# Optimization experiments

Measured on AMD Instinct MI355X. Metric: run time of the kernel, lower is better.

Reference implementation:

```python
import jax, jax.numpy as jnp
import numpy as np

B, T, P, H = 64, 64, 32, 256  # batch, seq_len, num_series, hidden


def setup_inputs() -> dict:
    key = jax.random.key(0)
    ks = jax.random.split(key, 16)
    s = 0.05  # weight init scale (keeps gates unsaturated, like PyTorch's 1/sqrt(H) init)
    return {
        'X': jax.random.normal(ks[0], (B, T, P), dtype=jnp.float32),
        'eps': jax.random.normal(ks[1], (1, B, H), dtype=jnp.float32),
        'W_ih_enc': jax.random.normal(ks[2], (3 * H, P), dtype=jnp.float32) * s,
        'W_hh_enc': jax.random.normal(ks[3], (3 * H, H), dtype=jnp.float32) * s,
        'b_ih_enc': jax.random.normal(ks[4], (3 * H,), dtype=jnp.float32) * s,
        'b_hh_enc': jax.random.normal(ks[5], (3 * H,), dtype=jnp.float32) * s,
        'fc_mu_w': jax.random.normal(ks[6], (H, H), dtype=jnp.float32) * s,
        'fc_mu_b': jax.random.normal(ks[7], (H,), dtype=jnp.float32) * s,
        'fc_std_w': jax.random.normal(ks[8], (H, H), dtype=jnp.float32) * s,
        'fc_std_b': jax.random.normal(ks[9], (H,), dtype=jnp.float32) * s,
        'W_ih_dec': jax.random.normal(ks[10], (P, 3 * H, P), dtype=jnp.float32) * s,
        'W_hh_dec': jax.random.normal(ks[11], (P, 3 * H, H), dtype=jnp.float32) * s,
        'b_ih_dec': jax.random.normal(ks[12], (P, 3 * H), dtype=jnp.float32) * s,
        'b_hh_dec': jax.random.normal(ks[13], (P, 3 * H), dtype=jnp.float32) * s,
        'lin_w': jax.random.normal(ks[14], (P, 1, H), dtype=jnp.float32) * s,
        'lin_b': jax.random.normal(ks[15], (P, 1), dtype=jnp.float32) * s,
    }


def _gru_scan(x_seq, h0, Wih, Whh, bih, bhh):
    """PyTorch-convention GRU over x_seq [B,T,in] with h0 [B,H]. Returns (h_last, hs [B,T,H])."""
    Hh = Whh.shape[1]
    # batch the input projection for all timesteps at once
    gi = jnp.einsum('bti,gi->btg', x_seq, Wih) + bih  # [B,T,3H]

    def step(h, gi_t):
        gh = h @ Whh.T + bhh
        r = jax.nn.sigmoid(gi_t[:, :Hh] + gh[:, :Hh])
        zg = jax.nn.sigmoid(gi_t[:, Hh:2 * Hh] + gh[:, Hh:2 * Hh])
        n = jnp.tanh(gi_t[:, 2 * Hh:] + r * gh[:, 2 * Hh:])
        h_new = (1.0 - zg) * n + zg * h
        return h_new, h_new

    h_last, hs = jax.lax.scan(step, h0, jnp.swapaxes(gi, 0, 1))
    return h_last, jnp.swapaxes(hs, 0, 1)


def reference(X, eps, W_ih_enc, W_hh_enc, b_ih_enc, b_hh_enc,
              fc_mu_w, fc_mu_b, fc_std_w, fc_std_b,
              W_ih_dec, W_hh_dec, b_ih_dec, b_hh_dec, lin_w, lin_b):
    # phase=0, mode='train'. Padded Xp = cat(zeros[:, :1], X); Xp[:,1:11] == X[:,0:10].
    Bb = X.shape[0]
    h0 = jnp.zeros((Bb, H), X.dtype)
    h_t, _ = _gru_scan(X[:, 0:10, :], h0, W_ih_enc, W_hh_enc, b_ih_enc, b_hh_enc)  # [B,H]
    mu = h_t @ fc_mu_w.T + fc_mu_b
    log_var = h_t @ fc_std_w.T + fc_std_b
    sigma = jnp.exp(0.5 * log_var)
    z = mu + sigma * eps[0]  # reparameterization; eps plays the role of torch.randn

    # decoder input: cat(Xp[:,0:1], Xp[:,11:-1]) == cat(zeros step, X[:,10:T-1])  -> [B, T-10, P]
    dec_in = jnp.concatenate([jnp.zeros_like(X[:, :1, :]), X[:, 10:-1, :]], axis=1)

    def one_series(Wih, Whh, bih, bhh, lw, lb):
        _, hs = _gru_scan(dec_in, z, Wih, Whh, bih, bhh)  # [B, T-10, H]
        return jnp.einsum('bth,oh->bto', hs, lw) + lb     # [B, T-10, 1]

    # connection is all-ones -> every decoder sees the full dec_in; vmap over stacked params
    pred = jax.vmap(one_series)(W_ih_dec, W_hh_dec, b_ih_dec, b_hh_dec, lin_w, lin_b)  # [P,B,T-10,1]
    return pred, log_var[None], mu[None]
```

## Files before the change

kernel.cpp:

```cpp
#include <hip/hip_runtime.h>

typedef unsigned int u32;
typedef unsigned short u16;
typedef __attribute__((ext_vector_type(8))) short short8;
typedef __attribute__((ext_vector_type(4))) float f32x4;

#define DEV static __device__ __forceinline__

DEV float b2f(u16 v){ union{u32 u; float f;} c; c.u = ((u32)v) << 16; return c.f; }
DEV u16 f2b(float f){ union{float ff; u32 u;} c; c.ff = f; return (u16)((c.u + 0x7fffu + ((c.u >> 16) & 1u)) >> 16); }
DEV float sigm(float x){ return 1.f/(1.f + __expf(-x)); }
DEV float tanh_(float x){ float e = __expf(-2.f*x); return (1.f-e)/(1.f+e); }

#define SER_STRIDE 221184

#define BLDS_U16 (48*3*64*8)
#define HA_U16   (2*2048)
#define XAB_U16  (2*256)
#define LWF_U16  256
#define SMEM_BYTES ((BLDS_U16 + HA_U16 + XAB_U16 + LWF_U16)*2)

DEV int hxi(int m, int c){ return (((c>>5)*32) + (((c>>3)&3)*8) + m)*8 + (c&7); }

__global__ __launch_bounds__(256) void pack_kernel(
    const float* __restrict__ WihD, const float* __restrict__ WhhD,
    const float* __restrict__ WihE, const float* __restrict__ WhhE,
    u16* __restrict__ wsB)
{
  const int ps = blockIdx.y;
  const int f  = blockIdx.x*4 + (threadIdx.x >> 6);
  const int n0 = f / 9, k = f - n0*9;
  const int lane = threadIdx.x & 63;
  const int n = lane & 15, q = lane >> 4;
  const int row = n0*16 + n;
  const float* Whh = (ps < 32) ? WhhD + ps*196608 : WhhE;
  const float* Wih = (ps < 32) ? WihD + ps*24576  : WihE;
  const float* src = (k < 8) ? (Whh + row*256 + k*32 + q*8) : (Wih + row*32 + q*8);
  u32 wd[4];
  #pragma unroll
  for (int j = 0; j < 4; ++j) {
    u16 lo = f2b(src[2*j]);
    u16 hi = f2b(src[2*j+1]);
    wd[j] = (u32)lo | ((u32)hi << 16);
  }
  *(uint4*)(wsB + (((size_t)ps*432 + f)*64 + lane)*8) = make_uint4(wd[0], wd[1], wd[2], wd[3]);
}

template<int NSTEPS, bool IS_DEC>
DEV void gru_body(u16* hA, u16* xA, u16* Blds, u16* lwfc,
                  const u16* __restrict__ Bp,
                  const float* __restrict__ bihP, const float* __restrict__ bhhP,
                  const float* __restrict__ X, const float* __restrict__ z0,
                  const float* __restrict__ lwp, const float* __restrict__ lbp,
                  float* __restrict__ predp, int b0)
{
  const int tid = threadIdx.x;
  const int w = tid >> 6, lane = tid & 63;
  const int n = lane & 15, q = lane >> 4;
  const int isel  = q >> 1;
  const int mbase = (q & 1) * 4;
  const int colS  = (2*w + isel)*16 + n;

  for (int idx = tid; idx < (HA_U16 + XAB_U16)/2; idx += 512)
    ((u32*)hA)[idx] = 0;
  __syncthreads();

  if (IS_DEC) {
    const int m = tid >> 6, c0 = (tid*4) & 255;
    float4 v = *(const float4*)&z0[(b0+m)*256 + c0];
    const int base = hxi(m, c0);
    hA[base]   = f2b(v.x); hA[base+1] = f2b(v.y);
    hA[base+2] = f2b(v.z); hA[base+3] = f2b(v.w);
  } else if (tid < 256) {
    const int m = tid >> 5, c = tid & 31;
    xA[((c>>3)*8 + m)*8 + (c&7)] = f2b(X[(b0+m)*2048 + c]);
  }
  if (IS_DEC && tid < 256)
    lwfc[tid] = f2b(lwp[tid]);

  #pragma unroll
  for (int r = 0; r < 18; ++r) {
    const int g = r*512 + tid;
    const int frag = g >> 6, e = g & 63;
    const int nt = frag / 3, kk = frag - nt*3;
    ((uint4*)Blds)[g] = ((const uint4*)Bp)[((size_t)nt*9 + 6 + kk)*64 + e];
  }

  short8 Bres[36];
  #pragma unroll
  for (int i = 0; i < 2; ++i)
    #pragma unroll
    for (int g = 0; g < 3; ++g)
      #pragma unroll
      for (int k = 0; k < 6; ++k)
        Bres[(i*3+g)*6 + k] =
          *(const short8*)(Bp + (((size_t)(g*16 + 2*w + i)*9 + k)*64 + lane)*8);
  #pragma unroll
  for (int r = 0; r < 36; ++r)
    asm volatile("" : "+v"(Bres[r]));

  const float brS  = bihP[colS]     + bhhP[colS];
  const float bzS  = bihP[256+colS] + bhhP[256+colS];
  const float bnxS = bihP[512+colS];
  const float bnhS = bhhP[512+colS];
  const float lb = IS_DEC ? lbp[0] : 0.f;

  float hold[4];
  #pragma unroll
  for (int rr = 0; rr < 4; ++rr)
    hold[rr] = IS_DEC ? b2f(f2b(z0[(b0 + mbase + rr)*256 + colS])) : 0.f;

  const int wbase = hxi(mbase, colS);
  __syncthreads();

  #pragma unroll 1
  for (int t = 0; t < NSTEPS; ++t) {
    const int par = t & 1;
    u16* hP = hA + par*2048;

    float xv = 0.f;
    const bool doX = (t+1 < NSTEPS) && (tid < 256);
    const int xm = tid >> 5, xc = tid & 31;
    if (doX) xv = X[(b0+xm)*2048 + (IS_DEC ? (t+10) : (t+1))*32 + xc];

    short8 af[9];
    #pragma unroll
    for (int k0 = 0; k0 < 8; ++k0)
      af[k0] = *(const short8*)&hP[(k0*32 + q*8 + (n&7))*8];
    af[8] = *(const short8*)&xA[par*256 + (q*8 + (n&7))*8];

    if (IS_DEC && w == 0 && t > 0) {
      f32x4 lp = {0,0,0,0};
      #pragma unroll
      for (int k0 = 0; k0 < 8; ++k0) {
        const short8 lf = *(const short8*)&lwfc[(k0*4 + q)*8];
        lp = __builtin_amdgcn_mfma_f32_16x16x32_bf16(af[k0], lf, lp, 0,0,0);
      }
      if (n == 0 && q < 2) {
        #pragma unroll
        for (int rr = 0; rr < 4; ++rr)
          predp[(b0 + q*4 + rr)*54 + (t-1)] = lp[rr] + lb;
      }
    }

    if (doX) xA[(par^1)*256 + ((xc>>3)*8 + xm)*8 + (xc&7)] = f2b(xv);

    f32x4 accr[2], accz[2], accnh[2], accnx[2];
    #pragma unroll
    for (int i = 0; i < 2; ++i) {
      const int ntr = 2*w + i, ntz = 16 + 2*w + i, ntn = 32 + 2*w + i;
      f32x4 ar={0,0,0,0}, az={0,0,0,0}, anh={0,0,0,0}, anx={0,0,0,0};
      const short8 b6r = *(const short8*)&Blds[((ntr*3+0)*64+lane)*8];
      const short8 b7r = *(const short8*)&Blds[((ntr*3+1)*64+lane)*8];
      const short8 b8r = *(const short8*)&Blds[((ntr*3+2)*64+lane)*8];
      const short8 b6z = *(const short8*)&Blds[((ntz*3+0)*64+lane)*8];
      const short8 b7z = *(const short8*)&Blds[((ntz*3+1)*64+lane)*8];
      const short8 b8z = *(const short8*)&Blds[((ntz*3+2)*64+lane)*8];
      const short8 b6n = *(const short8*)&Blds[((ntn*3+0)*64+lane)*8];
      const short8 b7n = *(const short8*)&Blds[((ntn*3+1)*64+lane)*8];
      const short8 b8n = *(const short8*)&Blds[((ntn*3+2)*64+lane)*8];
      #pragma unroll
      for (int k = 0; k < 6; ++k) {
        ar  = __builtin_amdgcn_mfma_f32_16x16x32_bf16(af[k], Bres[(i*3+0)*6+k], ar, 0,0,0);
        az  = __builtin_amdgcn_mfma_f32_16x16x32_bf16(af[k], Bres[(i*3+1)*6+k], az, 0,0,0);
        anh = __builtin_amdgcn_mfma_f32_16x16x32_bf16(af[k], Bres[(i*3+2)*6+k], anh, 0,0,0);
      }
      ar  = __builtin_amdgcn_mfma_f32_16x16x32_bf16(af[6], b6r, ar, 0,0,0);
      ar  = __builtin_amdgcn_mfma_f32_16x16x32_bf16(af[7], b7r, ar, 0,0,0);
      ar  = __builtin_amdgcn_mfma_f32_16x16x32_bf16(af[8], b8r, ar, 0,0,0);
      az  = __builtin_amdgcn_mfma_f32_16x16x32_bf16(af[6], b6z, az, 0,0,0);
      az  = __builtin_amdgcn_mfma_f32_16x16x32_bf16(af[7], b7z, az, 0,0,0);
      az  = __builtin_amdgcn_mfma_f32_16x16x32_bf16(af[8], b8z, az, 0,0,0);
      anh = __builtin_amdgcn_mfma_f32_16x16x32_bf16(af[6], b6n, anh, 0,0,0);
      anh = __builtin_amdgcn_mfma_f32_16x16x32_bf16(af[7], b7n, anh, 0,0,0);
      anx = __builtin_amdgcn_mfma_f32_16x16x32_bf16(af[8], b8n, anx, 0,0,0);
      accr[i] = ar; accz[i] = az; accnh[i] = anh; accnx[i] = anx;
    }

    u16* hW = hA + (par^1)*2048;
    #pragma unroll
    for (int rr = 0; rr < 4; ++rr) {
      const float r1  = __shfl_xor(accr[1][rr],  32, 64);
      const float z1  = __shfl_xor(accz[1][rr],  32, 64);
      const float nh1 = __shfl_xor(accnh[1][rr], 32, 64);
      const float nx1 = __shfl_xor(accnx[1][rr], 32, 64);
      const float arv  = (q >= 2) ? r1  : accr[0][rr];
      const float azv  = (q >= 2) ? z1  : accz[0][rr];
      const float anhv = (q >= 2) ? nh1 : accnh[0][rr];
      const float anxv = (q >= 2) ? nx1 : accnx[0][rr];
      const float rg = sigm(arv + brS);
      const float zg = sigm(azv + bzS);
      const float nv = tanh_(anxv + bnxS + rg*(anhv + bnhS));
      const float hn = (1.f - zg)*nv + zg*hold[rr];
      const u16 hb = f2b(hn);
      hold[rr] = b2f(hb);
      hW[wbase + rr*8] = hb;
    }
    __syncthreads();
  }

  if (IS_DEC && w == 0) {
    const u16* hF = hA + (NSTEPS&1)*2048;
    f32x4 lp = {0,0,0,0};
    #pragma unroll
    for (int k0 = 0; k0 < 8; ++k0) {
      const short8 a = *(const short8*)&hF[(k0*32 + q*8 + (n&7))*8];
      const short8 lf = *(const short8*)&lwfc[(k0*4 + q)*8];
      lp = __builtin_amdgcn_mfma_f32_16x16x32_bf16(a, lf, lp, 0,0,0);
    }
    if (n == 0 && q < 2) {
      #pragma unroll
      for (int rr = 0; rr < 4; ++rr)
        predp[(b0 + q*4 + rr)*54 + (NSTEPS-1)] = lp[rr] + lb;
    }
  }
}

__global__ __launch_bounds__(512, 2) void enc_lat(
    const u16* __restrict__ wsB,
    const float* __restrict__ bih, const float* __restrict__ bhh,
    const float* __restrict__ X,
    const float* __restrict__ Wmu, const float* __restrict__ bmu,
    const float* __restrict__ Wsd, const float* __restrict__ bsd,
    const float* __restrict__ eps,
    float* __restrict__ z, float* __restrict__ out_lv, float* __restrict__ out_mu)
{
  extern __shared__ char smem[];
  u16* Blds = (u16*)smem;
  u16* hA   = Blds + BLDS_U16;
  u16* xA   = hA + HA_U16;
  u16* lwfc = xA + XAB_U16;
  const int b0 = blockIdx.y * 8;
  gru_body<10, false>(hA, xA, Blds, lwfc, wsB + (size_t)32*SER_STRIDE,
                      bih, bhh, X, nullptr, nullptr, nullptr, nullptr, b0);
  __syncthreads();
  const int tid = threadIdx.x;
  const int j = tid & 255, half = tid >> 8;
  float am[4] = {0,0,0,0}, as[4] = {0,0,0,0};
  const float* wmrow = Wmu + j*256;
  const float* wsrow = Wsd + j*256;
  const u16* hF = hA + ((10)&1)*2048;
  #pragma unroll 2
  for (int c0 = 0; c0 < 256; c0 += 8) {
    float4 wm0 = *(const float4*)&wmrow[c0];
    float4 wm1 = *(const float4*)&wmrow[c0+4];
    float4 ws0 = *(const float4*)&wsrow[c0];
    float4 ws1 = *(const float4*)&wsrow[c0+4];
    #pragma unroll
    for (int mm = 0; mm < 4; ++mm) {
      const u16* hp = &hF[hxi(half*4 + mm, c0)];
      float h0x=b2f(hp[0]), h0y=b2f(hp[1]), h0z=b2f(hp[2]), h0w=b2f(hp[3]);
      float h1x=b2f(hp[4]), h1y=b2f(hp[5]), h1z=b2f(hp[6]), h1w=b2f(hp[7]);
      am[mm] += wm0.x*h0x + wm0.y*h0y + wm0.z*h0z + wm0.w*h0w
              + wm1.x*h1x + wm1.y*h1y + wm1.z*h1z + wm1.w*h1w;
      as[mm] += ws0.x*h0x + ws0.y*h0y + ws0.z*h0z + ws0.w*h0w
              + ws1.x*h1x + ws1.y*h1y + ws1.z*h1z + ws1.w*h1w;
    }
  }
  #pragma unroll
  for (int mm = 0; mm < 4; ++mm) {
    const int b = b0 + half*4 + mm;
    const float mu = am[mm] + bmu[j];
    const float lv = as[mm] + bsd[j];
    const float zv = mu + __expf(0.5f*lv) * eps[b*256 + j];
    z[b*256 + j]      = zv;
    out_lv[b*256 + j] = lv;
    out_mu[b*256 + j] = mu;
  }
}

__global__ __launch_bounds__(512, 2) void dec_mfma(
    const u16* __restrict__ wsB,
    const float* __restrict__ bih, const float* __restrict__ bhh,
    const float* __restrict__ X, const float* __restrict__ z,
    const float* __restrict__ lin_w, const float* __restrict__ lin_b,
    float* __restrict__ pred)
{
  extern __shared__ char smem[];
  u16* Blds = (u16*)smem;
  u16* hA   = Blds + BLDS_U16;
  u16* xA   = hA + HA_U16;
  u16* lwfc = xA + XAB_U16;
  const int p = blockIdx.x;
  const int b0 = blockIdx.y * 8;
  gru_body<54, true>(hA, xA, Blds, lwfc, wsB + (size_t)p*SER_STRIDE,
                     bih + p*768, bhh + p*768, X, z,
                     lin_w + p*256, lin_b + p, pred + p*3456, b0);
}

extern "C" void kernel_launch(void* const* d_in, const int* in_sizes, int n_in,
                              void* d_out, int out_size, void* d_ws, size_t ws_size,
                              hipStream_t stream) {
  const float* X        = (const float*)d_in[0];
  const float* eps      = (const float*)d_in[1];
  const float* Wih_enc  = (const float*)d_in[2];
  const float* Whh_enc  = (const float*)d_in[3];
  const float* bih_enc  = (const float*)d_in[4];
  const float* bhh_enc  = (const float*)d_in[5];
  const float* fc_mu_w  = (const float*)d_in[6];
  const float* fc_mu_b  = (const float*)d_in[7];
  const float* fc_std_w = (const float*)d_in[8];
  const float* fc_std_b = (const float*)d_in[9];
  const float* Wih_dec  = (const float*)d_in[10];
  const float* Whh_dec  = (const float*)d_in[11];
  const float* bih_dec  = (const float*)d_in[12];
  const float* bhh_dec  = (const float*)d_in[13];
  const float* lin_w    = (const float*)d_in[14];
  const float* lin_b    = (const float*)d_in[15];

  float* out    = (float*)d_out;
  float* pred   = out;
  float* out_lv = out + 110592;
  float* out_mu = out + 126976;

  u16*   wsB = (u16*)d_ws;
  float* z   = (float*)((char*)d_ws + (size_t)33*SER_STRIDE*2);

  (void)hipFuncSetAttribute((const void*)enc_lat,
      hipFuncAttributeMaxDynamicSharedMemorySize, SMEM_BYTES);
  (void)hipFuncSetAttribute((const void*)dec_mfma,
      hipFuncAttributeMaxDynamicSharedMemorySize, SMEM_BYTES);

  pack_kernel<<<dim3(108, 33), 256, 0, stream>>>(Wih_dec, Whh_dec, Wih_enc, Whh_enc, wsB);
  enc_lat<<<dim3(1, 8), 512, SMEM_BYTES, stream>>>(
      wsB, bih_enc, bhh_enc, X,
      fc_mu_w, fc_mu_b, fc_std_w, fc_std_b, eps, z, out_lv, out_mu);
  dec_mfma<<<dim3(32, 8), 512, SMEM_BYTES, stream>>>(
      wsB, bih_dec, bhh_dec, X, z, lin_w, lin_b, pred);
}
```

Before: 280.4 us.

## Fuse pack, encoder and decoder into one cooperative kernel with grid syncs

Replaces the three launches (weight packing, encoder+latent, decoder) with a single cooperative kernel of 256 blocks. Every block packs its own slice of the weights, then grid-syncs. Non-encoder blocks stage their decoder weights into LDS and registers while the 8 encoder blocks run the encoder GRU and latent projection, and a second grid sync follows. This removes launch gaps and overlaps the decoder weight staging with the encoder. In exchange it adds two grid-wide barriers and relies on all 256 blocks being co-resident, at two 512-thread blocks per CU.

```diff
diff --git a/kernel.cpp b/kernel.cpp
--- a/kernel.cpp
+++ b/kernel.cpp
@@ -1,4 +1,7 @@
 #include <hip/hip_runtime.h>
+#include <hip/hip_cooperative_groups.h>
+
+namespace cg = cooperative_groups;
 
 typedef unsigned int u32;
 typedef unsigned short u16;
@@ -22,19 +25,12 @@
 
 DEV int hxi(int m, int c){ return (((c>>5)*32) + (((c>>3)&3)*8) + m)*8 + (c&7); }
 
-__global__ __launch_bounds__(256) void pack_kernel(
-    const float* __restrict__ WihD, const float* __restrict__ WhhD,
-    const float* __restrict__ WihE, const float* __restrict__ WhhE,
-    u16* __restrict__ wsB)
-{
-  const int ps = blockIdx.y;
-  const int f  = blockIdx.x*4 + (threadIdx.x >> 6);
+DEV void pack_one(const float* __restrict__ Wih, const float* __restrict__ Whh,
+                  int f, int lane, u16* __restrict__ dstSer)
+{
   const int n0 = f / 9, k = f - n0*9;
-  const int lane = threadIdx.x & 63;
   const int n = lane & 15, q = lane >> 4;
   const int row = n0*16 + n;
-  const float* Whh = (ps < 32) ? WhhD + ps*196608 : WhhE;
-  const float* Wih = (ps < 32) ? WihD + ps*24576  : WihE;
   const float* src = (k < 8) ? (Whh + row*256 + k*32 + q*8) : (Wih + row*32 + q*8);
   u32 wd[4];
   #pragma unroll
@@ -43,16 +39,38 @@
     u16 hi = f2b(src[2*j+1]);
     wd[j] = (u32)lo | ((u32)hi << 16);
   }
-  *(uint4*)(wsB + (((size_t)ps*432 + f)*64 + lane)*8) = make_uint4(wd[0], wd[1], wd[2], wd[3]);
+  *(uint4*)(dstSer + ((size_t)f*64 + lane)*8) = make_uint4(wd[0], wd[1], wd[2], wd[3]);
+}
+
+DEV void stage_weights(const u16* __restrict__ Bp, u16* Blds, short8* Bres, int tid)
+{
+  const int w = tid >> 6, lane = tid & 63;
+  #pragma unroll
+  for (int r = 0; r < 18; ++r) {
+    const int g = r*512 + tid;
+    const int frag = g >> 6, e = g & 63;
+    const int nt = frag / 3, kk = frag - nt*3;
+    ((uint4*)Blds)[g] = ((const uint4*)Bp)[((size_t)nt*9 + 6 + kk)*64 + e];
+  }
+  #pragma unroll
+  for (int i = 0; i < 2; ++i)
+    #pragma unroll
+    for (int g = 0; g < 3; ++g)
+      #pragma unroll
+      for (int k = 0; k < 6; ++k)
+        Bres[(i*3+g)*6 + k] =
+          *(const short8*)(Bp + (((size_t)(g*16 + 2*w + i)*9 + k)*64 + lane)*8);
+  #pragma unroll
+  for (int r = 0; r < 36; ++r)
+    asm volatile("" : "+v"(Bres[r]));
 }
 
 template<int NSTEPS, bool IS_DEC>
-DEV void gru_body(u16* hA, u16* xA, u16* Blds, u16* lwfc,
-                  const u16* __restrict__ Bp,
-                  const float* __restrict__ bihP, const float* __restrict__ bhhP,
-                  const float* __restrict__ X, const float* __restrict__ z0,
-                  const float* __restrict__ lwp, const float* __restrict__ lbp,
-                  float* __restrict__ predp, int b0)
+DEV void gru_run(u16* hA, u16* xA, u16* lwfc, u16* Blds, const short8* Bres,
+                 const float* __restrict__ bihP, const float* __restrict__ bhhP,
+                 const float* __restrict__ X, const float* __restrict__ z0,
+                 const float* __restrict__ lwp, const float* __restrict__ lbp,
+                 float* __restrict__ predp, int b0)
 {
   const int tid = threadIdx.x;
   const int w = tid >> 6, lane = tid & 63;
@@ -61,8 +79,8 @@
   const int mbase = (q & 1) * 4;
   const int colS  = (2*w + isel)*16 + n;
 
-  for (int idx = tid; idx < (HA_U16 + XAB_U16)/2; idx += 512)
-    ((u32*)hA)[idx] = 0;
+  ((u32*)hA)[tid] = 0; ((u32*)hA)[tid + 512] = 0;
+  if (tid < 128) ((u32*)xA)[tid] = 0;
   __syncthreads();
 
   if (IS_DEC) {
@@ -71,33 +89,11 @@
     const int base = hxi(m, c0);
     hA[base]   = f2b(v.x); hA[base+1] = f2b(v.y);
     hA[base+2] = f2b(v.z); hA[base+3] = f2b(v.w);
+    if (tid < 256) lwfc[tid] = f2b(lwp[tid]);
   } else if (tid < 256) {
     const int m = tid >> 5, c = tid & 31;
     xA[((c>>3)*8 + m)*8 + (c&7)] = f2b(X[(b0+m)*2048 + c]);
   }
-  if (IS_DEC && tid < 256)
-    lwfc[tid] = f2b(lwp[tid]);
-
-  #pragma unroll
-  for (int r = 0; r < 18; ++r) {
-    const int g = r*512 + tid;
-    const int frag = g >> 6, e = g & 63;
-    const int nt = frag / 3, kk = frag - nt*3;
-    ((uint4*)Blds)[g] = ((const uint4*)Bp)[((size_t)nt*9 + 6 + kk)*64 + e];
-  }
-
-  short8 Bres[36];
-  #pragma unroll
-  for (int i = 0; i < 2; ++i)
-    #pragma unroll
-    for (int g = 0; g < 3; ++g)
-      #pragma unroll
-      for (int k = 0; k < 6; ++k)
-        Bres[(i*3+g)*6 + k] =
-          *(const short8*)(Bp + (((size_t)(g*16 + 2*w + i)*9 + k)*64 + lane)*8);
-  #pragma unroll
-  for (int r = 0; r < 36; ++r)
-    asm volatile("" : "+v"(Bres[r]));
 
   const float brS  = bihP[colS]     + bhhP[colS];
   const float bzS  = bihP[256+colS] + bhhP[256+colS];
@@ -216,30 +212,18 @@
   }
 }
 
-__global__ __launch_bounds__(512, 2) void enc_lat(
-    const u16* __restrict__ wsB,
-    const float* __restrict__ bih, const float* __restrict__ bhh,
-    const float* __restrict__ X,
-    const float* __restrict__ Wmu, const float* __restrict__ bmu,
-    const float* __restrict__ Wsd, const float* __restrict__ bsd,
-    const float* __restrict__ eps,
-    float* __restrict__ z, float* __restrict__ out_lv, float* __restrict__ out_mu)
-{
-  extern __shared__ char smem[];
-  u16* Blds = (u16*)smem;
-  u16* hA   = Blds + BLDS_U16;
-  u16* xA   = hA + HA_U16;
-  u16* lwfc = xA + XAB_U16;
-  const int b0 = blockIdx.y * 8;
-  gru_body<10, false>(hA, xA, Blds, lwfc, wsB + (size_t)32*SER_STRIDE,
-                      bih, bhh, X, nullptr, nullptr, nullptr, nullptr, b0);
-  __syncthreads();
-  const int tid = threadIdx.x;
+DEV void latent(const u16* hA,
+                const float* __restrict__ Wmu, const float* __restrict__ bmu,
+                const float* __restrict__ Wsd, const float* __restrict__ bsd,
+                const float* __restrict__ eps,
+                float* __restrict__ z, float* __restrict__ out_lv,
+                float* __restrict__ out_mu, int b0, int tid)
+{
   const int j = tid & 255, half = tid >> 8;
   float am[4] = {0,0,0,0}, as[4] = {0,0,0,0};
   const float* wmrow = Wmu + j*256;
   const float* wsrow = Wsd + j*256;
-  const u16* hF = hA + ((10)&1)*2048;
+  const u16* hF = hA;
   #pragma unroll 2
   for (int c0 = 0; c0 < 256; c0 += 8) {
     float4 wm0 = *(const float4*)&wmrow[c0];
@@ -269,23 +253,63 @@
   }
 }
 
-__global__ __launch_bounds__(512, 2) void dec_mfma(
-    const u16* __restrict__ wsB,
-    const float* __restrict__ bih, const float* __restrict__ bhh,
-    const float* __restrict__ X, const float* __restrict__ z,
+__global__ __launch_bounds__(512, 2) void fused(
+    const float* __restrict__ X, const float* __restrict__ eps,
+    const float* __restrict__ WihE, const float* __restrict__ WhhE,
+    const float* __restrict__ bihE, const float* __restrict__ bhhE,
+    const float* __restrict__ Wmu, const float* __restrict__ bmu,
+    const float* __restrict__ Wsd, const float* __restrict__ bsd,
+    const float* __restrict__ WihD, const float* __restrict__ WhhD,
+    const float* __restrict__ bihD, const float* __restrict__ bhhD,
     const float* __restrict__ lin_w, const float* __restrict__ lin_b,
-    float* __restrict__ pred)
+    u16* __restrict__ wsB, float* __restrict__ z,
+    float* __restrict__ pred, float* __restrict__ out_lv, float* __restrict__ out_mu)
 {
   extern __shared__ char smem[];
   u16* Blds = (u16*)smem;
   u16* hA   = Blds + BLDS_U16;
   u16* xA   = hA + HA_U16;
   u16* lwfc = xA + XAB_U16;
-  const int p = blockIdx.x;
-  const int b0 = blockIdx.y * 8;
-  gru_body<54, true>(hA, xA, Blds, lwfc, wsB + (size_t)p*SER_STRIDE,
-                     bih + p*768, bhh + p*768, X, z,
-                     lin_w + p*256, lin_b + p, pred + p*3456, b0);
+  const int gid = blockIdx.x;
+  const int p = gid & 31, s = gid >> 5, b0 = s*8;
+  const int tid = threadIdx.x;
+
+  {
+    const int fbase = s*54;
+    u16* dst = wsB + (size_t)p*SER_STRIDE;
+    const float* Wih = WihD + p*24576;
+    const float* Whh = WhhD + p*196608;
+    for (int it = tid; it < 54*64; it += 512)
+      pack_one(Wih, Whh, fbase + (it>>6), it & 63, dst);
+    if (gid >= 248) {
+      const int fb2 = (gid - 248)*54;
+      u16* dstE = wsB + (size_t)32*SER_STRIDE;
+      for (int it = tid; it < 54*64; it += 512)
+        pack_one(WihE, WhhE, fb2 + (it>>6), it & 63, dstE);
+    }
+  }
+  __threadfence();
+  cg::this_grid().sync();
+
+  short8 Bres[36];
+  if (gid < 8) {
+    stage_weights(wsB + (size_t)32*SER_STRIDE, Blds, Bres, tid);
+    gru_run<10, false>(hA, xA, lwfc, Blds, Bres, bihE, bhhE, X,
+                       nullptr, nullptr, nullptr, nullptr, gid*8);
+    __syncthreads();
+    latent(hA, Wmu, bmu, Wsd, bsd, eps, z, out_lv, out_mu, gid*8, tid);
+  } else {
+    stage_weights(wsB + (size_t)p*SER_STRIDE, Blds, Bres, tid);
+  }
+  __threadfence();
+  cg::this_grid().sync();
+
+  if (gid < 8)
+    stage_weights(wsB + (size_t)p*SER_STRIDE, Blds, Bres, tid);
+
+  gru_run<54, true>(hA, xA, lwfc, Blds, Bres,
+                    bihD + p*768, bhhD + p*768, X, z,
+                    lin_w + p*256, lin_b + p, pred + p*3456, b0);
 }
 
 extern "C" void kernel_launch(void* const* d_in, const int* in_sizes, int n_in,
@@ -316,15 +340,17 @@
   u16*   wsB = (u16*)d_ws;
   float* z   = (float*)((char*)d_ws + (size_t)33*SER_STRIDE*2);
 
-  (void)hipFuncSetAttribute((const void*)enc_lat,
+  (void)hipFuncSetAttribute((const void*)fused,
       hipFuncAttributeMaxDynamicSharedMemorySize, SMEM_BYTES);
-  (void)hipFuncSetAttribute((const void*)dec_mfma,
-      hipFuncAttributeMaxDynamicSharedMemorySize, SMEM_BYTES);
-
-  pack_kernel<<<dim3(108, 33), 256, 0, stream>>>(Wih_dec, Whh_dec, Wih_enc, Whh_enc, wsB);
-  enc_lat<<<dim3(1, 8), 512, SMEM_BYTES, stream>>>(
-      wsB, bih_enc, bhh_enc, X,
-      fc_mu_w, fc_mu_b, fc_std_w, fc_std_b, eps, z, out_lv, out_mu);
-  dec_mfma<<<dim3(32, 8), 512, SMEM_BYTES, stream>>>(
-      wsB, bih_dec, bhh_dec, X, z, lin_w, lin_b, pred);
-}
+
+  void* args[] = {
+    (void*)&X, (void*)&eps,
+    (void*)&Wih_enc, (void*)&Whh_enc, (void*)&bih_enc, (void*)&bhh_enc,
+    (void*)&fc_mu_w, (void*)&fc_mu_b, (void*)&fc_std_w, (void*)&fc_std_b,
+    (void*)&Wih_dec, (void*)&Whh_dec, (void*)&bih_dec, (void*)&bhh_dec,
+    (void*)&lin_w, (void*)&lin_b,
+    (void*)&wsB, (void*)&z, (void*)&pred, (void*)&out_lv, (void*)&out_mu
+  };
+  (void)hipLaunchCooperativeKernel((const void*)fused, dim3(256), dim3(512),
+                                   args, SMEM_BYTES, stream);
+}
```

After: 455.9 us. 62.6% more time.

## Preload all decoder inputs to LDS and keep more weight fragments in registers

Applied to the files above, without the earlier changes.

Before the recurrence starts, the inputs for every timestep are converted to bf16 and staged in LDS, so the per-step global load and double-buffered input write go away. One more K-slice of the recurrent weights moves from LDS into registers (42 fragments instead of 36), which shrinks the LDS weight buffer. The MFMA loop is restructured to load each A fragment once and feed all six accumulators plus the output-projection MFMA. This raises register pressure, which could cause spills at two blocks per CU, and enlarges LDS use for the input staging.

```diff
diff --git a/kernel.cpp b/kernel.cpp
--- a/kernel.cpp
+++ b/kernel.cpp
@@ -14,11 +14,11 @@
 
 #define SER_STRIDE 221184
 
-#define BLDS_U16 (48*3*64*8)
+#define BLDS_U16 (48*2*64*8)
 #define HA_U16   (2*2048)
-#define XAB_U16  (2*256)
+#define XALL_U16 (54*256)
 #define LWF_U16  256
-#define SMEM_BYTES ((BLDS_U16 + HA_U16 + XAB_U16 + LWF_U16)*2)
+#define SMEM_BYTES ((BLDS_U16 + HA_U16 + XALL_U16 + LWF_U16)*2)
 
 DEV int hxi(int m, int c){ return (((c>>5)*32) + (((c>>3)&3)*8) + m)*8 + (c&7); }
 
@@ -47,7 +47,7 @@
 }
 
 template<int NSTEPS, bool IS_DEC>
-DEV void gru_body(u16* hA, u16* xA, u16* Blds, u16* lwfc,
+DEV void gru_body(u16* hA, u16* xall, u16* Blds, u16* lwfc,
                   const u16* __restrict__ Bp,
                   const float* __restrict__ bihP, const float* __restrict__ bhhP,
                   const float* __restrict__ X, const float* __restrict__ z0,
@@ -61,8 +61,7 @@
   const int mbase = (q & 1) * 4;
   const int colS  = (2*w + isel)*16 + n;
 
-  for (int idx = tid; idx < (HA_U16 + XAB_U16)/2; idx += 512)
-    ((u32*)hA)[idx] = 0;
+  ((u32*)hA)[tid] = 0; ((u32*)hA)[tid + 512] = 0;
   __syncthreads();
 
   if (IS_DEC) {
@@ -71,32 +70,38 @@
     const int base = hxi(m, c0);
     hA[base]   = f2b(v.x); hA[base+1] = f2b(v.y);
     hA[base+2] = f2b(v.z); hA[base+3] = f2b(v.w);
-  } else if (tid < 256) {
-    const int m = tid >> 5, c = tid & 31;
-    xA[((c>>3)*8 + m)*8 + (c&7)] = f2b(X[(b0+m)*2048 + c]);
-  }
-  if (IS_DEC && tid < 256)
-    lwfc[tid] = f2b(lwp[tid]);
-
-  #pragma unroll
-  for (int r = 0; r < 18; ++r) {
+    if (tid < 256) lwfc[tid] = f2b(lwp[tid]);
+  }
+
+  for (int idx = tid; idx < NSTEPS*256; idx += 512) {
+    const int t = idx >> 8, r = idx & 255;
+    const int c = ((r >> 6) << 3) | (r & 7);
+    const int m = (r >> 3) & 7;
+    float v;
+    if (IS_DEC) v = (t == 0) ? 0.f : X[(b0+m)*2048 + (t+9)*32 + c];
+    else        v = X[(b0+m)*2048 + t*32 + c];
+    xall[idx] = f2b(v);
+  }
+
+  #pragma unroll
+  for (int r = 0; r < 12; ++r) {
     const int g = r*512 + tid;
     const int frag = g >> 6, e = g & 63;
-    const int nt = frag / 3, kk = frag - nt*3;
-    ((uint4*)Blds)[g] = ((const uint4*)Bp)[((size_t)nt*9 + 6 + kk)*64 + e];
-  }
-
-  short8 Bres[36];
+    const int nt = frag >> 1, kk = frag & 1;
+    ((uint4*)Blds)[g] = ((const uint4*)Bp)[((size_t)nt*9 + 7 + kk)*64 + e];
+  }
+
+  short8 Bres[42];
   #pragma unroll
   for (int i = 0; i < 2; ++i)
     #pragma unroll
     for (int g = 0; g < 3; ++g)
       #pragma unroll
-      for (int k = 0; k < 6; ++k)
-        Bres[(i*3+g)*6 + k] =
+      for (int k = 0; k < 7; ++k)
+        Bres[(i*3+g)*7 + k] =
           *(const short8*)(Bp + (((size_t)(g*16 + 2*w + i)*9 + k)*64 + lane)*8);
   #pragma unroll
-  for (int r = 0; r < 36; ++r)
+  for (int r = 0; r < 42; ++r)
     asm volatile("" : "+v"(Bres[r]));
 
   const float brS  = bihP[colS]     + bhhP[colS];
@@ -111,87 +116,98 @@
     hold[rr] = IS_DEC ? b2f(f2b(z0[(b0 + mbase + rr)*256 + colS])) : 0.f;
 
   const int wbase = hxi(mbase, colS);
+  const int nt0 = 2*w,      nt1 = 2*w + 1;
   __syncthreads();
 
   #pragma unroll 1
   for (int t = 0; t < NSTEPS; ++t) {
     const int par = t & 1;
-    u16* hP = hA + par*2048;
-
-    float xv = 0.f;
-    const bool doX = (t+1 < NSTEPS) && (tid < 256);
-    const int xm = tid >> 5, xc = tid & 31;
-    if (doX) xv = X[(b0+xm)*2048 + (IS_DEC ? (t+10) : (t+1))*32 + xc];
-
-    short8 af[9];
-    #pragma unroll
-    for (int k0 = 0; k0 < 8; ++k0)
-      af[k0] = *(const short8*)&hP[(k0*32 + q*8 + (n&7))*8];
-    af[8] = *(const short8*)&xA[par*256 + (q*8 + (n&7))*8];
-
-    if (IS_DEC && w == 0 && t > 0) {
-      f32x4 lp = {0,0,0,0};
-      #pragma unroll
-      for (int k0 = 0; k0 < 8; ++k0) {
-        const short8 lf = *(const short8*)&lwfc[(k0*4 + q)*8];
-        lp = __builtin_amdgcn_mfma_f32_16x16x32_bf16(af[k0], lf, lp, 0,0,0);
+    const u16* hP = hA + par*2048;
+    const int arow = (q*8 + (n&7))*8;
+
+    f32x4 ar0={0,0,0,0}, az0={0,0,0,0}, anh0={0,0,0,0}, anx0={0,0,0,0};
+    f32x4 ar1={0,0,0,0}, az1={0,0,0,0}, anh1={0,0,0,0}, anx1={0,0,0,0};
+    f32x4 lp ={0,0,0,0};
+    const bool doLin = IS_DEC && (w == 0) && (t > 0);
+
+    #pragma unroll
+    for (int k = 0; k < 7; ++k) {
+      const short8 a = *(const short8*)&hP[(k*32)*8 + arow];
+      ar0  = __builtin_amdgcn_mfma_f32_16x16x32_bf16(a, Bres[0*7+k],  ar0, 0,0,0);
+      az0  = __builtin_amdgcn_mfma_f32_16x16x32_bf16(a, Bres[1*7+k],  az0, 0,0,0);
+      anh0 = __builtin_amdgcn_mfma_f32_16x16x32_bf16(a, Bres[2*7+k],  anh0,0,0,0);
+      ar1  = __builtin_amdgcn_mfma_f32_16x16x32_bf16(a, Bres[3*7+k],  ar1, 0,0,0);
+      az1  = __builtin_amdgcn_mfma_f32_16x16x32_bf16(a, Bres[4*7+k],  az1, 0,0,0);
+      anh1 = __builtin_amdgcn_mfma_f32_16x16x32_bf16(a, Bres[5*7+k],  anh1,0,0,0);
+      if (doLin) {
+        const short8 lf = *(const short8*)&lwfc[(k*4 + q)*8];
+        lp = __builtin_amdgcn_mfma_f32_16x16x32_bf16(a, lf, lp, 0,0,0);
       }
-      if (n == 0 && q < 2) {
-        #pragma unroll
-        for (int rr = 0; rr < 4; ++rr)
-          predp[(b0 + q*4 + rr)*54 + (t-1)] = lp[rr] + lb;
+    }
+    {
+      const short8 a = *(const short8*)&hP[(7*32)*8 + arow];
+      #pragma unroll
+      for (int i = 0; i < 2; ++i) {
+        const int nti = 2*w + i;
+        const short8 b7r = *(const short8*)&Blds[(((nti     )*2+0)*64+lane)*8];
+        const short8 b7z = *(const short8*)&Blds[(((16+nti  )*2+0)*64+lane)*8];
+        const short8 b7n = *(const short8*)&Blds[(((32+nti  )*2+0)*64+lane)*8];
+        if (i == 0) {
+          ar0  = __builtin_amdgcn_mfma_f32_16x16x32_bf16(a, b7r, ar0, 0,0,0);
+          az0  = __builtin_amdgcn_mfma_f32_16x16x32_bf16(a, b7z, az0, 0,0,0);
+          anh0 = __builtin_amdgcn_mfma_f32_16x16x32_bf16(a, b7n, anh0,0,0,0);
+        } else {
+          ar1  = __builtin_amdgcn_mfma_f32_16x16x32_bf16(a, b7r, ar1, 0,0,0);
+          az1  = __builtin_amdgcn_mfma_f32_16x16x32_bf16(a, b7z, az1, 0,0,0);
+          anh1 = __builtin_amdgcn_mfma_f32_16x16x32_bf16(a, b7n, anh1,0,0,0);
+        }
       }
-    }
-
-    if (doX) xA[(par^1)*256 + ((xc>>3)*8 + xm)*8 + (xc&7)] = f2b(xv);
-
-    f32x4 accr[2], accz[2], accnh[2], accnx[2];
-    #pragma unroll
-    for (int i = 0; i < 2; ++i) {
-      const int ntr = 2*w + i, ntz = 16 + 2*w + i, ntn = 32 + 2*w + i;
-      f32x4 ar={0,0,0,0}, az={0,0,0,0}, anh={0,0,0,0}, anx={0,0,0,0};
-      const short8 b6r = *(const short8*)&Blds[((ntr*3+0)*64+lane)*8];
-      const short8 b7r = *(const short8*)&Blds[((ntr*3+1)*64+lane)*8];
-      const short8 b8r = *(const short8*)&Blds[((ntr*3+2)*64+lane)*8];
-      const short8 b6z = *(const short8*)&Blds[((ntz*3+0)*64+lane)*8];
-      const short8 b7z = *(const short8*)&Blds[((ntz*3+1)*64+lane)*8];
-      const short8 b8z = *(const short8*)&Blds[((ntz*3+2)*64+lane)*8];
-      const short8 b6n = *(const short8*)&Blds[((ntn*3+0)*64+lane)*8];
-      const short8 b7n = *(const short8*)&Blds[((ntn*3+1)*64+lane)*8];
-      const short8 b8n = *(const short8*)&Blds[((ntn*3+2)*64+lane)*8];
-      #pragma unroll
-      for (int k = 0; k < 6; ++k) {
-        ar  = __builtin_amdgcn_mfma_f32_16x16x32_bf16(af[k], Bres[(i*3+0)*6+k], ar, 0,0,0);
-        az  = __builtin_amdgcn_mfma_f32_16x16x32_bf16(af[k], Bres[(i*3+1)*6+k], az, 0,0,0);
-        anh = __builtin_amdgcn_mfma_f32_16x16x32_bf16(af[k], Bres[(i*3+2)*6+k], anh, 0,0,0);
+      if (doLin) {
+        const short8 lf = *(const short8*)&lwfc[(7*4 + q)*8];
+        lp = __builtin_amdgcn_mfma_f32_16x16x32_bf16(a, lf, lp, 0,0,0);
       }
-      ar  = __builtin_amdgcn_mfma_f32_16x16x32_bf16(af[6], b6r, ar, 0,0,0);
-      ar  = __builtin_amdgcn_mfma_f32_16x16x32_bf16(af[7], b7r, ar, 0,0,0);
-      ar  = __builtin_amdgcn_mfma_f32_16x16x32_bf16(af[8], b8r, ar, 0,0,0);
-      az  = __builtin_amdgcn_mfma_f32_16x16x32_bf16(af[6], b6z, az, 0,0,0);
-      az  = __builtin_amdgcn_mfma_f32_16x16x32_bf16(af[7], b7z, az, 0,0,0);
-      az  = __builtin_amdgcn_mfma_f32_16x16x32_bf16(af[8], b8z, az, 0,0,0);
-      anh = __builtin_amdgcn_mfma_f32_16x16x32_bf16(af[6], b6n, anh, 0,0,0);
-      anh = __builtin_amdgcn_mfma_f32_16x16x32_bf16(af[7], b7n, anh, 0,0,0);
-      anx = __builtin_amdgcn_mfma_f32_16x16x32_bf16(af[8], b8n, anx, 0,0,0);
-      accr[i] = ar; accz[i] = az; accnh[i] = anh; accnx[i] = anx;
+    }
+    {
+      const short8 a = *(const short8*)&xall[t*256 + arow];
+      #pragma unroll
+      for (int i = 0; i < 2; ++i) {
+        const int nti = 2*w + i;
+        const short8 b8r = *(const short8*)&Blds[(((nti     )*2+1)*64+lane)*8];
+        const short8 b8z = *(const short8*)&Blds[(((16+nti  )*2+1)*64+lane)*8];
+        const short8 b8n = *(const short8*)&Blds[(((32+nti  )*2+1)*64+lane)*8];
+        if (i == 0) {
+          ar0  = __builtin_amdgcn_mfma_f32_16x16x32_bf16(a, b8r, ar0, 0,0,0);
+          az0  = __builtin_amdgcn_mfma_f32_16x16x32_bf16(a, b8z, az0, 0,0,0);
+          anx0 = __builtin_amdgcn_mfma_f32_16x16x32_bf16(a, b8n, anx0,0,0,0);
+        } else {
+          ar1  = __builtin_amdgcn_mfma_f32_16x16x32_bf16(a, b8r, ar1, 0,0,0);
+          az1  = __builtin_amdgcn_mfma_f32_16x16x32_bf16(a, b8z, az1, 0,0,0);
+          anx1 = __builtin_amdgcn_mfma_f32_16x16x32_bf16(a, b8n, anx1,0,0,0);
+        }
+      }
+    }
+
+    if (doLin && n == 0 && q < 2) {
+      #pragma unroll
+      for (int rr = 0; rr < 4; ++rr)
+        predp[(b0 + q*4 + rr)*54 + (t-1)] = lp[rr] + lb;
     }
 
     u16* hW = hA + (par^1)*2048;
     #pragma unroll
     for (int rr = 0; rr < 4; ++rr) {
-      const float r1  = __shfl_xor(accr[1][rr],  32, 64);
-      const float z1  = __shfl_xor(accz[1][rr],  32, 64);
-      const float nh1 = __shfl_xor(accnh[1][rr], 32, 64);
-      const float nx1 = __shfl_xor(accnx[1][rr], 32, 64);
-      const float arv  = (q >= 2) ? r1  : accr[0][rr];
-      const float azv  = (q >= 2) ? z1  : accz[0][rr];
-      const float anhv = (q >= 2) ? nh1 : accnh[0][rr];
-      const float anxv = (q >= 2) ? nx1 : accnx[0][rr];
+      const float r1  = __shfl_xor(ar1[rr],  32, 64);
+      const float z1  = __shfl_xor(az1[rr],  32, 64);
+      const float nh1 = __shfl_xor(anh1[rr], 32, 64);
+      const float nx1 = __shfl_xor(anx1[rr], 32, 64);
+      const float arv  = (q >= 2) ? r1  : ar0[rr];
+      const float azv  = (q >= 2) ? z1  : az0[rr];
+      const float anhv = (q >= 2) ? nh1 : anh0[rr];
+      const float anxv = (q >= 2) ? nx1 : anx0[rr];
       const float rg = sigm(arv + brS);
       const float zg = sigm(azv + bzS);
       const float nv = tanh_(anxv + bnxS + rg*(anhv + bnhS));
-      const float hn = (1.f - zg)*nv + zg*hold[rr];
+      const float hn = nv + zg*(hold[rr] - nv);
       const u16 hb = f2b(hn);
       hold[rr] = b2f(hb);
       hW[wbase + rr*8] = hb;
@@ -228,10 +244,10 @@
   extern __shared__ char smem[];
   u16* Blds = (u16*)smem;
   u16* hA   = Blds + BLDS_U16;
-  u16* xA   = hA + HA_U16;
-  u16* lwfc = xA + XAB_U16;
+  u16* xall = hA + HA_U16;
+  u16* lwfc = xall + XALL_U16;
   const int b0 = blockIdx.y * 8;
-  gru_body<10, false>(hA, xA, Blds, lwfc, wsB + (size_t)32*SER_STRIDE,
+  gru_body<10, false>(hA, xall, Blds, lwfc, wsB + (size_t)32*SER_STRIDE,
                       bih, bhh, X, nullptr, nullptr, nullptr, nullptr, b0);
   __syncthreads();
   const int tid = threadIdx.x;
@@ -239,7 +255,7 @@
   float am[4] = {0,0,0,0}, as[4] = {0,0,0,0};
   const float* wmrow = Wmu + j*256;
   const float* wsrow = Wsd + j*256;
-  const u16* hF = hA + ((10)&1)*2048;
+  const u16* hF = hA;
   #pragma unroll 2
   for (int c0 = 0; c0 < 256; c0 += 8) {
     float4 wm0 = *(const float4*)&wmrow[c0];
@@ -279,11 +295,11 @@
   extern __shared__ char smem[];
   u16* Blds = (u16*)smem;
   u16* hA   = Blds + BLDS_U16;
-  u16* xA   = hA + HA_U16;
-  u16* lwfc = xA + XAB_U16;
+  u16* xall = hA + HA_U16;
+  u16* lwfc = xall + XALL_U16;
   const int p = blockIdx.x;
   const int b0 = blockIdx.y * 8;
-  gru_body<54, true>(hA, xA, Blds, lwfc, wsB + (size_t)p*SER_STRIDE,
+  gru_body<54, true>(hA, xall, Blds, lwfc, wsB + (size_t)p*SER_STRIDE,
                      bih + p*768, bhh + p*768, X, z,
                      lin_w + p*256, lin_b + p, pred + p*3456, b0);
 }
```

Measured after the change: 292.8 us. +4.4%, slower.
